# Kernel optimization log

Measured on AMD Instinct MI355X. Metric: run time of the kernel, lower is better.

The kernel has to match this reference:

```python
import jax, jax.numpy as jnp
import numpy as np

B, S, T = 8, 2048, 128  # batch, seq_len, token_embedding_dim (== dep_transformed_dim, required by source bug)


def setup_inputs() -> dict:
    key = jax.random.key(0)
    k1, k2, k3, k4, k5, k6, k7 = jax.random.split(key, 7)
    sT = 1.0 / np.sqrt(T)
    sS = 1.0 / np.sqrt(S)
    return {
        "token_embeddings": jax.random.normal(k1, (B, S, T), jnp.float32),
        "dep_embeddings": jax.random.normal(k2, (B, S, T), jnp.float32),  # dead input (source bug), kept for fidelity
        "dep_heads": jax.random.randint(k3, (B, S), 0, S, jnp.int32),
        # composition_transform = Bilinear(T, T, T): weight [T_out, T_in1, T_in2], bias [T_out]
        "W_comp": jax.random.uniform(k4, (T, T, T), jnp.float32, -sT, sT),
        "b_comp": jax.random.uniform(k5, (T,), jnp.float32, -sT, sT),
        # reduction_transform = Linear(S, 1)
        "w_red": jax.random.uniform(k6, (1, S), jnp.float32, -sS, sS),
        "b_red": jax.random.uniform(k7, (1,), jnp.float32, -sS, sS),
    }


def reference(token_embeddings, dep_embeddings, dep_heads, W_comp, b_comp, w_red, b_red):
    # Faithful to source semantics (including the bug where dep_transform output is
    # discarded and tanh is applied to token_embeddings instead):
    #   dense[b,i,j,:] = tanh( bilinear(token[b,j], mask(i==heads[b,j]) * tanh(token[b,j])) )
    #   out[b,i,t]     = sum_j w_red[j] * dense[b,i,j,t] + b_red
    # Where mask is zero, bilinear collapses to its bias, so we never materialize
    # the [B,S,S,T] tensor: compute the 'active' value per token j and scatter-add
    # the delta vs. the bias-only baseline into row i = dep_heads[b,j].
    h = jnp.tanh(token_embeddings)                                   # [B,S,T]
    val = jnp.einsum('bsp,tpq,bsq->bst', token_embeddings, W_comp, h) + b_comp  # [B,S,T]
    act = jnp.tanh(val)                                              # active (masked-in) values
    base_val = jnp.tanh(b_comp)                                      # [T] value where mask is zero
    w = w_red[0]                                                     # [S], reduction weights over j
    base = jnp.sum(w) * base_val + b_red[0]                          # [T] bias-only row
    delta = w[None, :, None] * (act - base_val)                      # [B,S,T]
    b_idx = jnp.arange(token_embeddings.shape[0])[:, None]           # [B,1]
    out = base + jnp.zeros_like(act).at[b_idx, dep_heads].add(delta) # scatter over head rows
    return out
```

## Files before the change

kernel.cpp:

```cpp
#include <hip/hip_runtime.h>
#include <hip/hip_fp16.h>
#include <math.h>

#define S_LEN 2048
#define T_DIM 128
#define BM 128
#define TN 64
#define NBLK 256
#define TOKR 132

typedef _Float16 half8 __attribute__((ext_vector_type(8)));
typedef _Float16 half4t __attribute__((ext_vector_type(4)));
typedef float floatx16 __attribute__((ext_vector_type(16)));

__device__ __forceinline__ float tanh_fast(float x) {
  return 1.0f - __fdividef(2.0f, 1.0f + __expf(2.0f * x));
}

__global__ __launch_bounds__(256) void prep_kernel(
    const float* __restrict__ W, const float* __restrict__ w_red,
    const float* __restrict__ b_comp, const float* __restrict__ b_red,
    _Float16* __restrict__ W16f, float* __restrict__ out) {
  const int blk = blockIdx.x;
  const int tid = threadIdx.x;
  if (blk < 1024) {
    const int t = blk >> 3;
    const int qh = (blk >> 2) & 1;
    const int it = blk & 3;
    const int tc = t >> 5, tl = t & 31;
    const int e8 = it * 256 + tid;
    const int p = e8 >> 3;
    const int q = qh * 64 + (e8 & 7) * 8;
    const float* src = W + (size_t)t * 16384 + (size_t)p * 128 + q;
    const float4 v0 = *(const float4*)src;
    const float4 v1 = *(const float4*)(src + 4);
    half8 h;
    h[0] = (_Float16)v0.x; h[1] = (_Float16)v0.y;
    h[2] = (_Float16)v0.z; h[3] = (_Float16)v0.w;
    h[4] = (_Float16)v1.x; h[5] = (_Float16)v1.y;
    h[6] = (_Float16)v1.z; h[7] = (_Float16)v1.w;
    const int kc = q >> 4, lh2 = (q >> 3) & 1;
    *(half8*)(W16f + ((size_t)((p * 4 + tc) * 8 + kc)) * 512 + lh2 * 256 + tl * 8) = h;
  } else {
    __shared__ float red4[4];
    float part = 0.f;
#pragma unroll
    for (int i = 0; i < 8; ++i) part += w_red[i * 256 + tid];
#pragma unroll
    for (int off = 32; off > 0; off >>= 1) part += __shfl_down(part, off, 64);
    if ((tid & 63) == 0) red4[tid >> 6] = part;
    __syncthreads();
    const float Sw = red4[0] + red4[1] + red4[2] + red4[3];
    const float br = b_red[0];
    const size_t base = (size_t)(blk - 1024) * 1024 + (size_t)tid * 4;
    const int t0 = (int)(base & 127);
    float4 v;
    v.x = Sw * tanh_fast(b_comp[t0 + 0]) + br;
    v.y = Sw * tanh_fast(b_comp[t0 + 1]) + br;
    v.z = Sw * tanh_fast(b_comp[t0 + 2]) + br;
    v.w = Sw * tanh_fast(b_comp[t0 + 3]) + br;
    *(float4*)(out + base) = v;
  }
}

__global__ __launch_bounds__(512, 2) void main_kernel(
    const float* __restrict__ tok, const int* __restrict__ heads,
    const _Float16* __restrict__ W16f, const float* __restrict__ b_comp,
    const float* __restrict__ w_red, float* __restrict__ out) {
  __shared__ __align__(16) char smem[65536];
  _Float16* const tokT2 = (_Float16*)smem;
  float* const red0 = (float*)smem;
  float* const red1 = (float*)smem + BM * TN;

  const int tid = threadIdx.x;
  const int lane = tid & 63;
  const int kh = tid >> 6;
  const int l31 = lane & 31;
  const int lh = lane >> 5;
  const int blk = blockIdx.x;
  const int th = blk & 1;
  const int mb = blk >> 1;
  const int pstag = ((blk >> 3) * 4) & 127;
  const size_t tokbase = (size_t)mb * BM * T_DIM;

  int off[2];
#pragma unroll
  for (int tt = 0; tt < 2; ++tt)
    off[tt] = (((th * 2 + tt) * 8 + kh) << 9) + lane * 8;

  half8 bf0[2], bf1[2], bf2[2];
  half4t tk0, tk1, tk2;
  half8 aA[4], aB[4];
  half8 h16[4];

  auto loadB = [&](half8 (&bf)[2], int p) {
    const int pp = (p + pstag) & 127;
    const _Float16* wp = W16f + (size_t)pp * 16384;
    bf[0] = *(const half8*)(wp + off[0]);
    bf[1] = *(const half8*)(wp + off[1]);
  };
  auto loadT = [&](half4t& tk, int p) {
    const int pp = (p + pstag) & 127;
    const int col = (l31 * 4) ^ (((pp + (pp >> 3)) & 7) << 2);
    tk = *(const half4t*)(tokT2 + pp * TOKR + col);
  };
  auto build = [&](half8 (&a)[4], half4t tk) {
#pragma unroll
    for (int mh = 0; mh < 4; ++mh) a[mh] = h16[mh] * tk[mh];
  };

  loadB(bf0, 0);
  loadB(bf1, 1);

#pragma unroll
  for (int it = 0; it < 8; ++it) {
    const int f = it * 512 + tid;
    const int m = f >> 5;
    const int p0 = (f & 31) * 4;
    const float4 v = *(const float4*)(tok + tokbase + (size_t)m * 128 + p0);
    const int mi = (m & 31) * 4 + (m >> 5);
    const float vv[4] = {v.x, v.y, v.z, v.w};
#pragma unroll
    for (int jj = 0; jj < 4; ++jj) {
      const int p = p0 + jj;
      const int col = mi ^ (((p + (p >> 3)) & 7) << 2);
      tokT2[p * TOKR + col] = (_Float16)vv[jj];
    }
  }

#pragma unroll
  for (int mh = 0; mh < 4; ++mh) {
    const int m = mh * 32 + l31;
    const int q0 = kh * 16 + lh * 8;
    const float4 v0 = *(const float4*)(tok + tokbase + (size_t)m * 128 + q0);
    const float4 v1 = *(const float4*)(tok + tokbase + (size_t)m * 128 + q0 + 4);
    h16[mh][0] = (_Float16)tanh_fast(v0.x);
    h16[mh][1] = (_Float16)tanh_fast(v0.y);
    h16[mh][2] = (_Float16)tanh_fast(v0.z);
    h16[mh][3] = (_Float16)tanh_fast(v0.w);
    h16[mh][4] = (_Float16)tanh_fast(v1.x);
    h16[mh][5] = (_Float16)tanh_fast(v1.y);
    h16[mh][6] = (_Float16)tanh_fast(v1.z);
    h16[mh][7] = (_Float16)tanh_fast(v1.w);
  }

  floatx16 acc[4][2];
#pragma unroll
  for (int mh = 0; mh < 4; ++mh)
#pragma unroll
    for (int tt = 0; tt < 2; ++tt)
#pragma unroll
      for (int r = 0; r < 16; ++r) acc[mh][tt][r] = 0.f;

  __syncthreads();

  auto mfma8 = [&](half8 (&a)[4], half8 (&bf)[2]) {
    __builtin_amdgcn_s_setprio(1);
#pragma unroll
    for (int mh = 0; mh < 4; ++mh) {
      acc[mh][0] = __builtin_amdgcn_mfma_f32_32x32x16_f16(a[mh], bf[0], acc[mh][0], 0, 0, 0);
      acc[mh][1] = __builtin_amdgcn_mfma_f32_32x32x16_f16(a[mh], bf[1], acc[mh][1], 0, 0, 0);
    }
    __builtin_amdgcn_s_setprio(0);
  };

  loadT(tk0, 0);
  loadT(tk1, 1);
  build(aA, tk0);

#define SUBSTEP(BF_CUR, BF_PRE, TK_NXT, TK_PRE, A_CUR, A_NXT, K) \
  {                                                              \
    mfma8(A_CUR, BF_CUR);                                        \
    loadB(BF_PRE, (K) + 2);                                      \
    loadT(TK_PRE, (K) + 2);                                      \
    build(A_NXT, TK_NXT);                                        \
  }
  for (int p = 0; p < 126; p += 6) {
    SUBSTEP(bf0, bf2, tk1, tk2, aA, aB, p + 0);
    SUBSTEP(bf1, bf0, tk2, tk0, aB, aA, p + 1);
    SUBSTEP(bf2, bf1, tk0, tk1, aA, aB, p + 2);
    SUBSTEP(bf0, bf2, tk1, tk2, aB, aA, p + 3);
    SUBSTEP(bf1, bf0, tk2, tk0, aA, aB, p + 4);
    SUBSTEP(bf2, bf1, tk0, tk1, aB, aA, p + 5);
  }
#undef SUBSTEP
  mfma8(aA, bf0);
  build(aB, tk1);
  mfma8(aB, bf1);

  __syncthreads();
  {
    float* R = (kh & 1) ? red1 : red0;
    const int g = kh >> 1;
#pragma unroll
    for (int phase = 0; phase < 4; ++phase) {
      if (g == phase) {
#pragma unroll
        for (int mh = 0; mh < 4; ++mh)
#pragma unroll
          for (int tt = 0; tt < 2; ++tt) {
            const int t_loc = tt * 32 + l31;
#pragma unroll
            for (int r = 0; r < 16; ++r) {
              const int m_loc = mh * 32 + (r & 3) + 8 * (r >> 2) + 4 * lh;
              const int addr = m_loc * TN + t_loc;
              if (phase == 0) R[addr] = acc[mh][tt][r];
              else            R[addr] += acc[mh][tt][r];
            }
          }
      }
      __syncthreads();
    }
  }

  const int t_loc = tid & 63;
  const int mgrp = tid >> 6;
  const int t = th * 64 + t_loc;
  const float bc = b_comp[t];
  const float tb = tanh_fast(bc);
#pragma unroll 4
  for (int mi = 0; mi < 16; ++mi) {
    const int m_loc = mi * 8 + mgrp;
    const int gm = mb * BM + m_loc;
    const int head = heads[gm];
    const float wr = w_red[gm & 2047];
    const float v = red0[m_loc * TN + t_loc] + red1[m_loc * TN + t_loc] + bc;
    atomicAdd(out + ((size_t)(gm >> 11) * S_LEN + head) * T_DIM + t,
              wr * (tanh_fast(v) - tb));
  }
}

extern "C" void kernel_launch(void* const* d_in, const int* in_sizes, int n_in,
                              void* d_out, int out_size, void* d_ws, size_t ws_size,
                              hipStream_t stream) {
  const float* tok    = (const float*)d_in[0];
  const int*   heads  = (const int*)d_in[2];
  const float* W      = (const float*)d_in[3];
  const float* b_comp = (const float*)d_in[4];
  const float* w_red  = (const float*)d_in[5];
  const float* b_red  = (const float*)d_in[6];
  float* out = (float*)d_out;

  _Float16* W16f = (_Float16*)d_ws;

  prep_kernel<<<3072, 256, 0, stream>>>(W, w_red, b_comp, b_red, W16f, out);
  main_kernel<<<NBLK, 512, 0, stream>>>(tok, heads, W16f, b_comp, w_red, out);
}
```

Measured before the change: 151.0 us.

## Stream fp16 weight tiles through LDS with async global_load_lds triple buffering

Replaces direct per-wave register loads of the fp16 bilinear weight fragments with async global-to-LDS copies (global_load_lds) into a three-slot ring buffer, processing two p-steps per phase behind vmcnt waits and barriers. The A operand is now built inline within each MFMA cluster instead of being double-buffered in registers. The aim is to hide global memory latency and lower register pressure on the weight stream. In exchange, LDS use grows to about 130KB per block, which limits occupancy, and a block-wide barrier is added every phase.

```diff
diff --git a/kernel.cpp b/kernel.cpp
--- a/kernel.cpp
+++ b/kernel.cpp
@@ -8,13 +8,21 @@
 #define TN 64
 #define NBLK 256
 #define TOKR 132
+#define SLOT0 34816
 
 typedef _Float16 half8 __attribute__((ext_vector_type(8)));
 typedef _Float16 half4t __attribute__((ext_vector_type(4)));
 typedef float floatx16 __attribute__((ext_vector_type(16)));
+typedef unsigned int u32;
 
 __device__ __forceinline__ float tanh_fast(float x) {
   return 1.0f - __fdividef(2.0f, 1.0f + __expf(2.0f * x));
+}
+
+__device__ __forceinline__ void load_lds16(const void* g, void* l) {
+  __builtin_amdgcn_global_load_lds(
+      (const __attribute__((address_space(1))) u32*)g,
+      (__attribute__((address_space(3))) u32*)l, 16, 0, 0);
 }
 
 __global__ __launch_bounds__(256) void prep_kernel(
@@ -67,10 +75,10 @@
     const float* __restrict__ tok, const int* __restrict__ heads,
     const _Float16* __restrict__ W16f, const float* __restrict__ b_comp,
     const float* __restrict__ w_red, float* __restrict__ out) {
-  __shared__ __align__(16) char smem[65536];
+  __shared__ __align__(16) char smem[133120];
   _Float16* const tokT2 = (_Float16*)smem;
   float* const red0 = (float*)smem;
-  float* const red1 = (float*)smem + BM * TN;
+  float* const red1 = (float*)(smem + 32768);
 
   const int tid = threadIdx.x;
   const int lane = tid & 63;
@@ -83,34 +91,53 @@
   const int pstag = ((blk >> 3) * 4) & 127;
   const size_t tokbase = (size_t)mb * BM * T_DIM;
 
-  int off[2];
-#pragma unroll
-  for (int tt = 0; tt < 2; ++tt)
-    off[tt] = (((th * 2 + tt) * 8 + kh) << 9) + lane * 8;
-
-  half8 bf0[2], bf1[2], bf2[2];
-  half4t tk0, tk1, tk2;
-  half8 aA[4], aB[4];
+  char* const myslot = smem + SLOT0 + kh * 4096;
+  const char* const wsrc = (const char*)W16f + (size_t)lane * 16;
+
   half8 h16[4];
-
-  auto loadB = [&](half8 (&bf)[2], int p) {
-    const int pp = (p + pstag) & 127;
-    const _Float16* wp = W16f + (size_t)pp * 16384;
-    bf[0] = *(const half8*)(wp + off[0]);
-    bf[1] = *(const half8*)(wp + off[1]);
-  };
-  auto loadT = [&](half4t& tk, int p) {
-    const int pp = (p + pstag) & 127;
-    const int col = (l31 * 4) ^ (((pp + (pp >> 3)) & 7) << 2);
-    tk = *(const half4t*)(tokT2 + pp * TOKR + col);
-  };
-  auto build = [&](half8 (&a)[4], half4t tk) {
-#pragma unroll
-    for (int mh = 0; mh < 4; ++mh) a[mh] = h16[mh] * tk[mh];
-  };
-
-  loadB(bf0, 0);
-  loadB(bf1, 1);
+  floatx16 acc[4][2];
+
+  auto stage = [&](int ph, int s) {
+#pragma unroll
+    for (int i = 0; i < 2; ++i) {
+      const int pp = (ph * 2 + i + pstag) & 127;
+#pragma unroll
+      for (int tt = 0; tt < 2; ++tt) {
+        const size_t gb = ((size_t)((pp * 4 + th * 2 + tt) * 8 + kh)) * 1024;
+        load_lds16(wsrc + gb, myslot + s * 32768 + (i * 2 + tt) * 1024);
+      }
+    }
+  };
+  auto readBF = [&](half8 (&bf)[2][2], int s) {
+#pragma unroll
+    for (int i = 0; i < 2; ++i)
+#pragma unroll
+      for (int tt = 0; tt < 2; ++tt)
+        bf[i][tt] = *(const half8*)(myslot + s * 32768 + (i * 2 + tt) * 1024 + lane * 16);
+  };
+  auto readTK = [&](half4t (&tk)[2], int ph) {
+#pragma unroll
+    for (int i = 0; i < 2; ++i) {
+      const int pp = (ph * 2 + i + pstag) & 127;
+      const int col = (l31 * 4) ^ (((pp + (pp >> 3)) & 7) << 2);
+      tk[i] = *(const half4t*)(tokT2 + pp * TOKR + col);
+    }
+  };
+  auto cluster = [&](half8 (&bf)[2][2], half4t (&tk)[2]) {
+    __builtin_amdgcn_s_setprio(1);
+#pragma unroll
+    for (int i = 0; i < 2; ++i)
+#pragma unroll
+      for (int mh = 0; mh < 4; ++mh) {
+        half8 a = h16[mh] * tk[i][mh];
+        acc[mh][0] = __builtin_amdgcn_mfma_f32_32x32x16_f16(a, bf[i][0], acc[mh][0], 0, 0, 0);
+        acc[mh][1] = __builtin_amdgcn_mfma_f32_32x32x16_f16(a, bf[i][1], acc[mh][1], 0, 0, 0);
+      }
+    __builtin_amdgcn_s_setprio(0);
+  };
+
+  stage(0, 0);
+  stage(1, 1);
 
 #pragma unroll
   for (int it = 0; it < 8; ++it) {
@@ -144,7 +171,6 @@
     h16[mh][7] = (_Float16)tanh_fast(v1.w);
   }
 
-  floatx16 acc[4][2];
 #pragma unroll
   for (int mh = 0; mh < 4; ++mh)
 #pragma unroll
@@ -154,39 +180,39 @@
 
   __syncthreads();
 
-  auto mfma8 = [&](half8 (&a)[4], half8 (&bf)[2]) {
-    __builtin_amdgcn_s_setprio(1);
-#pragma unroll
-    for (int mh = 0; mh < 4; ++mh) {
-      acc[mh][0] = __builtin_amdgcn_mfma_f32_32x32x16_f16(a[mh], bf[0], acc[mh][0], 0, 0, 0);
-      acc[mh][1] = __builtin_amdgcn_mfma_f32_32x32x16_f16(a[mh], bf[1], acc[mh][1], 0, 0, 0);
-    }
-    __builtin_amdgcn_s_setprio(0);
-  };
-
-  loadT(tk0, 0);
-  loadT(tk1, 1);
-  build(aA, tk0);
-
-#define SUBSTEP(BF_CUR, BF_PRE, TK_NXT, TK_PRE, A_CUR, A_NXT, K) \
-  {                                                              \
-    mfma8(A_CUR, BF_CUR);                                        \
-    loadB(BF_PRE, (K) + 2);                                      \
-    loadT(TK_PRE, (K) + 2);                                      \
-    build(A_NXT, TK_NXT);                                        \
-  }
-  for (int p = 0; p < 126; p += 6) {
-    SUBSTEP(bf0, bf2, tk1, tk2, aA, aB, p + 0);
-    SUBSTEP(bf1, bf0, tk2, tk0, aB, aA, p + 1);
-    SUBSTEP(bf2, bf1, tk0, tk1, aA, aB, p + 2);
-    SUBSTEP(bf0, bf2, tk1, tk2, aB, aA, p + 3);
-    SUBSTEP(bf1, bf0, tk2, tk0, aA, aB, p + 4);
-    SUBSTEP(bf2, bf1, tk0, tk1, aB, aA, p + 5);
-  }
-#undef SUBSTEP
-  mfma8(aA, bf0);
-  build(aB, tk1);
-  mfma8(aB, bf1);
+  half8 bfA[2][2], bfB[2][2];
+  half4t tkA[2], tkB[2];
+  readBF(bfA, 0);
+  readTK(tkA, 0);
+
+#define PHASE(PH, S_STAGE, S_READ, BFC, TKC, BFN, TKN)   \
+  {                                                      \
+    stage((PH) + 2, S_STAGE);                            \
+    asm volatile("s_waitcnt vmcnt(4)" ::: "memory");     \
+    __builtin_amdgcn_s_barrier();                        \
+    __builtin_amdgcn_sched_barrier(0);                   \
+    readBF(BFN, S_READ);                                 \
+    readTK(TKN, (PH) + 1);                               \
+    cluster(BFC, TKC);                                   \
+  }
+  for (int ph = 0; ph < 60; ph += 6) {
+    PHASE(ph + 0, 2, 1, bfA, tkA, bfB, tkB);
+    PHASE(ph + 1, 0, 2, bfB, tkB, bfA, tkA);
+    PHASE(ph + 2, 1, 0, bfA, tkA, bfB, tkB);
+    PHASE(ph + 3, 2, 1, bfB, tkB, bfA, tkA);
+    PHASE(ph + 4, 0, 2, bfA, tkA, bfB, tkB);
+    PHASE(ph + 5, 1, 0, bfB, tkB, bfA, tkA);
+  }
+  PHASE(60, 2, 1, bfA, tkA, bfB, tkB);
+  PHASE(61, 0, 2, bfB, tkB, bfA, tkA);
+#undef PHASE
+  asm volatile("s_waitcnt vmcnt(0)" ::: "memory");
+  __builtin_amdgcn_s_barrier();
+  __builtin_amdgcn_sched_barrier(0);
+  readBF(bfB, 0);
+  readTK(tkB, 63);
+  cluster(bfA, tkA);
+  cluster(bfB, tkB);
 
   __syncthreads();
   {
```

New measurement: 154.3 us. 1.02x slower.
